# Optimization experiments

Measured on AMD Instinct MI355X. Metric: run time of the kernel, lower is better.

## Reference

```python
import jax, jax.numpy as jnp
import numpy as np

K = 11          # kernel_size
SIGMA = 1.5
CH = 3          # image channels


def _gaussian_kernel(ch):
    coords = jnp.arange(K, dtype=jnp.float32) - (K - 1) / 2
    g = jnp.exp(-coords ** 2 / (2 * SIGMA ** 2))
    g = g / g.sum()
    k2d = jnp.outer(g, g)                       # [K, K]
    return jnp.tile(k2d[None, None], (ch, 1, 1, 1))  # [C, 1, K, K] depthwise


def setup_inputs() -> dict:
    key = jax.random.key(0)
    kx, ky = jax.random.split(key)
    x = jax.random.normal(kx, (32, CH, 512, 512), dtype=jnp.float32)
    y = jax.random.normal(ky, (32, CH, 512, 512), dtype=jnp.float32)
    kernel = _gaussian_kernel(CH)
    return {"x": x, "y": y, "kernel": kernel}


def _blur(v, kernel):
    # depthwise 2D Gaussian blur, SAME padding (K odd)
    c = v.shape[1]
    pad = K // 2
    return jax.lax.conv_general_dilated(
        v, kernel, window_strides=(1, 1), padding=[(pad, pad), (pad, pad)],
        dimension_numbers=("NCHW", "OIHW", "NCHW"), feature_group_count=c)


def reference(x, y, kernel):
    C1 = 0.01 ** 2
    C2 = 0.03 ** 2
    mu_x = _blur(x, kernel)
    mu_y = _blur(y, kernel)
    sigma_x = _blur(x * x, kernel) - mu_x ** 2
    sigma_y = _blur(y * y, kernel) - mu_y ** 2
    sigma_xy = _blur(x * y, kernel) - mu_x * mu_y
    ssim_num = (2 * mu_x * mu_y + C1) * (2 * sigma_xy + C2)
    ssim_den = (mu_x ** 2 + mu_y ** 2 + C1) * (sigma_x + sigma_y + C2)
    ssim = ssim_num / (ssim_den + 1e-8)
    return ((1.0 - ssim) / 2.0).mean()
```

## Files before the change

kernel.cpp:

```cpp
#include <hip/hip_runtime.h>
#include <hip/hip_bf16.h>

#define IMG    512
#define KSZ    11
#define HALO   5
#define STRIP  64
#define PANEL  16
#define NSTEP  32
#define PAIRS  37
#define FSTR32 44
#define FROW   704
#define RSTR32 340

typedef short bf16x8 __attribute__((ext_vector_type(8)));
typedef float f32x4  __attribute__((ext_vector_type(4)));
union S8 { bf16x8 v; ushort u16[8]; uint u32[4]; };

__device__ __forceinline__ uint cvtpk(float lo, float hi) {
    uint r;
    asm("v_cvt_pk_bf16_f32 %0, %1, %2" : "=v"(r) : "v"(lo), "v"(hi));
    return r;
}
__device__ __forceinline__ float2 pk_mul(float2 a, float2 b) {
    float2 d;
    asm("v_pk_mul_f32 %0, %1, %2" : "=v"(d) : "v"(a), "v"(b));
    return d;
}
__device__ __forceinline__ ushort f2bf(float f) {
    union { __hip_bfloat16 h; ushort u; } c;
    c.h = __float2bfloat16(f);
    return c.u;
}


__global__ __launch_bounds__(256)
void dssim_mfma_kernel(const float* __restrict__ x,
                       const float* __restrict__ y,
                       const float* __restrict__ kern,
                       float* __restrict__ out)
{
    __shared__ float  sgf[16];
    __shared__ ushort gext[64];
    __shared__ uint   Fbuf32[5 * FROW];
    __shared__ uint   Ring32[24 * RSTR32];
    __shared__ float  wsum[4];

    const int tid = threadIdx.x;
    const int l   = tid & 63;
    const int wv  = tid >> 6;
    const int q   = l >> 4;
    const int cj  = l & 15;
    const int wcb = wv * 16 + cj;

    if (tid < KSZ) {
        float s = 0.f;
        #pragma unroll
        for (int j = 0; j < KSZ; ++j) s += kern[tid * KSZ + j];
        sgf[tid] = s;
    }
    for (int i = tid; i < 5 * FROW; i += 256) Fbuf32[i] = 0u;
    for (int i = tid; i < 3 * RSTR32; i += 256) Ring32[i] = 0u;
    __syncthreads();
    if (tid < 64) {
        const int d = tid - 16;
        gext[tid] = (d >= 0 && d < KSZ) ? f2bf(sgf[d]) : (ushort)0;
    }
    __syncthreads();

    S8 tgh, tgv;
    #pragma unroll
    for (int ii = 0; ii < 8; ++ii) {
        tgh.u16[ii] = gext[16 + q * 8 + ii - cj];
        tgv.u16[ii] = gext[15 + q * 8 + ii - cj];
    }

    const int plane  = blockIdx.z;
    const int cstrip = blockIdx.x * STRIP;
    const int base   = plane * (IMG * IMG);

    const int srow = tid >> 4;
    const int sp   = tid & 15;
    int gcol0[3], gcol1[3], wo[3];
    bool ok0[3], ok1[3];
    #pragma unroll
    for (int m = 0; m < 3; ++m) {
        const int p  = sp + 16 * m;
        const bool pa = (p < PAIRS);
        const int c0 = cstrip - HALO + 2 * p;
        gcol0[m] = c0;  gcol1[m] = c0 + 1;
        ok0[m] = pa && (c0 >= 0) && (c0 < IMG);
        ok1[m] = pa && (c0 + 1 >= 0) && (c0 + 1 < IMG);
        wo[m]  = srow * FSTR32 + p;
    }
    float2 px[3], py[3];

    auto prefetch = [&](int pn) {
        const int r    = pn * PANEL + srow;
        const bool rok = (r < IMG);
        const int rb   = base + r * IMG;
        #pragma unroll
        for (int m = 0; m < 3; ++m) {
            float a0 = 0.f, a1 = 0.f, b0 = 0.f, b1 = 0.f;
            if (rok && ok0[m]) { a0 = x[rb + gcol0[m]]; b0 = y[rb + gcol0[m]]; }
            if (rok && ok1[m]) { a1 = x[rb + gcol1[m]]; b1 = y[rb + gcol1[m]]; }
            px[m] = make_float2(a0, a1);
            py[m] = make_float2(b0, b1);
        }
    };
    auto commit = [&]() {
        #pragma unroll
        for (int m = 0; m < 3; ++m) {
            if (m < 2 || sp < PAIRS - 32) {
                const float2 vx = px[m], vy = py[m];
                const float2 xx = pk_mul(vx, vx);
                const float2 yy = pk_mul(vy, vy);
                const float2 xy = pk_mul(vx, vy);
                Fbuf32[0 * FROW + wo[m]] = cvtpk(vx.x, vx.y);
                Fbuf32[1 * FROW + wo[m]] = cvtpk(vy.x, vy.y);
                Fbuf32[2 * FROW + wo[m]] = cvtpk(xx.x, xx.y);
                Fbuf32[3 * FROW + wo[m]] = cvtpk(yy.x, yy.y);
                Fbuf32[4 * FROW + wo[m]] = cvtpk(xy.x, xy.y);
            }
        }
    };

    prefetch(0);
    commit();
    __syncthreads();

    const f32x4 z0 = {0.f, 0.f, 0.f, 0.f};
    const float C1 = 1e-4f, C2 = 9e-4f;
    const int aoff = cj * FSTR32 + wv * 8 + q * 4;
    float local = 0.f;
    int hb = 0, vb = 16;

    for (int t = 0; t <= NSTEP; ++t) {
        {
            int p0 = hb + 2 * q + 3;  if (p0 >= 24) p0 -= 24;
            int p1 = p0 + 1;          if (p1 >= 24) p1 -= 24;
            const int rw0 = p0 * RSTR32 + wcb;
            const int rw1 = p1 * RSTR32 + wcb;
            #pragma unroll
            for (int f = 0; f < 5; ++f) {
                S8 a;
                a.v = *(const bf16x8*)&Fbuf32[f * FROW + aoff];
                f32x4 d = __builtin_amdgcn_mfma_f32_16x16x32_bf16(a.v, tgh.v, z0, 0, 0, 0);
                Ring32[rw0 + f * 68] = cvtpk(d[0], d[1]);
                Ring32[rw1 + f * 68] = cvtpk(d[2], d[3]);
            }
        }

        if (t < NSTEP) prefetch(t + 1);

        __syncthreads();

        if (t >= 1) {
            int vr[4];
            #pragma unroll
            for (int ii = 0; ii < 4; ++ii) {
                int pp = vb + 4 * q + ii;  if (pp >= 24) pp -= 24;
                vr[ii] = pp * RSTR32 + wcb;
            }
            f32x4 vf[5];
            #pragma unroll
            for (int f = 0; f < 5; ++f) {
                S8 b;
                #pragma unroll
                for (int ii = 0; ii < 4; ++ii) b.u32[ii] = Ring32[vr[ii] + f * 68];
                vf[f] = __builtin_amdgcn_mfma_f32_16x16x32_bf16(tgv.v, b.v, z0, 0, 0, 0);
            }
            #pragma unroll
            for (int r = 0; r < 4; ++r) {
                const float mx  = vf[0][r], my  = vf[1][r];
                const float exx = vf[2][r], eyy = vf[3][r], exy = vf[4][r];
                const float sxv = fmaf(-mx, mx, exx);
                const float syv = fmaf(-my, my, eyy);
                const float sxy = fmaf(-mx, my, exy);
                const float num = fmaf(2.f, mx * my, C1) * fmaf(2.f, sxy, C2);
                const float den = fmaf(mx, mx, fmaf(my, my, C1)) * (sxv + syv + C2);
                const float ssim = __fdividef(num, den + 1e-8f);
                local += (1.f - ssim) * 0.5f;
            }
        }

        if (t < NSTEP) commit();
        __syncthreads();

        vb = hb;
        hb += 8;  if (hb >= 24) hb -= 24;
    }

    #pragma unroll
    for (int o = 32; o > 0; o >>= 1) local += __shfl_down(local, o, 64);
    if (l == 0) wsum[wv] = local;
    __syncthreads();
    if (tid == 0) {
        const float s = wsum[0] + wsum[1] + wsum[2] + wsum[3];
        atomicAdd(out, s * (1.f / 25165824.f));
    }
}

extern "C" void kernel_launch(void* const* d_in, const int* in_sizes, int n_in,
                              void* d_out, int out_size, void* d_ws, size_t ws_size,
                              hipStream_t stream)
{
    const float* x    = (const float*)d_in[0];
    const float* y    = (const float*)d_in[1];
    const float* kern = (const float*)d_in[2];
    float* out = (float*)d_out;

    hipMemsetAsync(out, 0, sizeof(float), stream);

    dim3 grid(IMG / STRIP, 1, 32 * 3);
    dssim_mfma_kernel<<<grid, 256, 0, stream>>>(x, y, kern, out);
}
```

Before: 81.54 us.

## Feed MFMA A-operand from registers via vector loads and split image rows in halves

Removes the Fbuf shared-memory staging buffer: each lane now loads 8 contiguous floats of x and y with 128-bit vector loads and builds the bf16 A-fragments for the horizontal MFMA directly in registers. The Gaussian tap offsets are shifted to match the new column mapping, which uses a strip start 8 columns earlier. The grid doubles along y so each block processes half the rows, with one overlapping panel to refill the vertical ring. This cuts LDS traffic and a sync-heavy commit phase and raises parallelism, at the cost of some redundant halo panel loads and changed edge handling; colok zeroes whole 8-column groups at image borders.

```diff
diff --git a/kernel.cpp b/kernel.cpp
--- a/kernel.cpp
+++ b/kernel.cpp
@@ -6,11 +6,8 @@
 #define HALO   5
 #define STRIP  64
 #define PANEL  16
-#define NSTEP  32
-#define PAIRS  37
-#define FSTR32 44
-#define FROW   704
-#define RSTR32 340
+#define RSTR32 330
+#define FOFF   66
 
 typedef short bf16x8 __attribute__((ext_vector_type(8)));
 typedef float f32x4  __attribute__((ext_vector_type(4)));
@@ -41,7 +38,6 @@
 {
     __shared__ float  sgf[16];
     __shared__ ushort gext[64];
-    __shared__ uint   Fbuf32[5 * FROW];
     __shared__ uint   Ring32[24 * RSTR32];
     __shared__ float  wsum[4];
 
@@ -58,11 +54,10 @@
         for (int j = 0; j < KSZ; ++j) s += kern[tid * KSZ + j];
         sgf[tid] = s;
     }
-    for (int i = tid; i < 5 * FROW; i += 256) Fbuf32[i] = 0u;
     for (int i = tid; i < 3 * RSTR32; i += 256) Ring32[i] = 0u;
     __syncthreads();
     if (tid < 64) {
-        const int d = tid - 16;
+        const int d = tid - 18;
         gext[tid] = (d >= 0 && d < KSZ) ? f2bf(sgf[d]) : (ushort)0;
     }
     __syncthreads();
@@ -70,91 +65,94 @@
     S8 tgh, tgv;
     #pragma unroll
     for (int ii = 0; ii < 8; ++ii) {
-        tgh.u16[ii] = gext[16 + q * 8 + ii - cj];
-        tgv.u16[ii] = gext[15 + q * 8 + ii - cj];
+        tgh.u16[ii] = gext[15 + q * 8 + ii - cj];
+        tgv.u16[ii] = gext[17 + q * 8 + ii - cj];
     }
 
     const int plane  = blockIdx.z;
+    const int half   = blockIdx.y;
     const int cstrip = blockIdx.x * STRIP;
     const int base   = plane * (IMG * IMG);
 
-    const int srow = tid >> 4;
-    const int sp   = tid & 15;
-    int gcol0[3], gcol1[3], wo[3];
-    bool ok0[3], ok1[3];
-    #pragma unroll
-    for (int m = 0; m < 3; ++m) {
-        const int p  = sp + 16 * m;
-        const bool pa = (p < PAIRS);
-        const int c0 = cstrip - HALO + 2 * p;
-        gcol0[m] = c0;  gcol1[m] = c0 + 1;
-        ok0[m] = pa && (c0 >= 0) && (c0 < IMG);
-        ok1[m] = pa && (c0 + 1 >= 0) && (c0 + 1 < IMG);
-        wo[m]  = srow * FSTR32 + p;
-    }
-    float2 px[3], py[3];
-
-    auto prefetch = [&](int pn) {
-        const int r    = pn * PANEL + srow;
-        const bool rok = (r < IMG);
-        const int rb   = base + r * IMG;
-        #pragma unroll
-        for (int m = 0; m < 3; ++m) {
-            float a0 = 0.f, a1 = 0.f, b0 = 0.f, b1 = 0.f;
-            if (rok && ok0[m]) { a0 = x[rb + gcol0[m]]; b0 = y[rb + gcol0[m]]; }
-            if (rok && ok1[m]) { a1 = x[rb + gcol1[m]]; b1 = y[rb + gcol1[m]]; }
-            px[m] = make_float2(a0, a1);
-            py[m] = make_float2(b0, b1);
+    const int  cb    = cstrip - 8 + 16 * wv + 8 * q;
+    const bool colok = (cb >= 0) && (cb + 8 <= IMG);
+    const float* xp  = x + base + cb;
+    const float* yp  = y + base + cb;
+
+    const int t0   = half ? 15 : 0;
+    const int t1   = half ? 32 : 16;
+    const int vmin = half ? 17 : 1;
+
+    f32x4 xa, xb, ya, yb;
+    auto load8 = [&](int t) {
+        const int r = t * PANEL + cj;
+        if (r < IMG && colok) {
+            const float* px = xp + r * IMG;
+            const float* py = yp + r * IMG;
+            xa = *(const f32x4*)px;  xb = *(const f32x4*)(px + 4);
+            ya = *(const f32x4*)py;  yb = *(const f32x4*)(py + 4);
+        } else {
+            const f32x4 zz = {0.f, 0.f, 0.f, 0.f};
+            xa = zz; xb = zz; ya = zz; yb = zz;
         }
     };
-    auto commit = [&]() {
-        #pragma unroll
-        for (int m = 0; m < 3; ++m) {
-            if (m < 2 || sp < PAIRS - 32) {
-                const float2 vx = px[m], vy = py[m];
-                const float2 xx = pk_mul(vx, vx);
-                const float2 yy = pk_mul(vy, vy);
-                const float2 xy = pk_mul(vx, vy);
-                Fbuf32[0 * FROW + wo[m]] = cvtpk(vx.x, vx.y);
-                Fbuf32[1 * FROW + wo[m]] = cvtpk(vy.x, vy.y);
-                Fbuf32[2 * FROW + wo[m]] = cvtpk(xx.x, xx.y);
-                Fbuf32[3 * FROW + wo[m]] = cvtpk(yy.x, yy.y);
-                Fbuf32[4 * FROW + wo[m]] = cvtpk(xy.x, xy.y);
-            }
-        }
-    };
-
-    prefetch(0);
-    commit();
-    __syncthreads();
+
+    load8(t0);
 
     const f32x4 z0 = {0.f, 0.f, 0.f, 0.f};
     const float C1 = 1e-4f, C2 = 9e-4f;
-    const int aoff = cj * FSTR32 + wv * 8 + q * 4;
     float local = 0.f;
-    int hb = 0, vb = 16;
-
-    for (int t = 0; t <= NSTEP; ++t) {
+    int hb = (8 * t0) % 24;
+
+    for (int t = t0; t <= t1; ++t) {
+        float2 x01 = {xa[0], xa[1]}, x23 = {xa[2], xa[3]};
+        float2 x45 = {xb[0], xb[1]}, x67 = {xb[2], xb[3]};
+        float2 y01 = {ya[0], ya[1]}, y23 = {ya[2], ya[3]};
+        float2 y45 = {yb[0], yb[1]}, y67 = {yb[2], yb[3]};
+        S8 fx, fy, fxx, fyy, fxy;
+        #pragma unroll
+        for (int w = 0; w < 4; ++w) {
+            const float2 xv = (w == 0) ? x01 : (w == 1) ? x23 : (w == 2) ? x45 : x67;
+            const float2 yv = (w == 0) ? y01 : (w == 1) ? y23 : (w == 2) ? y45 : y67;
+            const float2 xxv = pk_mul(xv, xv);
+            const float2 yyv = pk_mul(yv, yv);
+            const float2 xyv = pk_mul(xv, yv);
+            fx .u32[w] = cvtpk(xv.x,  xv.y);
+            fy .u32[w] = cvtpk(yv.x,  yv.y);
+            fxx.u32[w] = cvtpk(xxv.x, xxv.y);
+            fyy.u32[w] = cvtpk(yyv.x, yyv.y);
+            fxy.u32[w] = cvtpk(xyv.x, xyv.y);
+        }
+
+        if (t < t1) load8(t + 1);
+
         {
             int p0 = hb + 2 * q + 3;  if (p0 >= 24) p0 -= 24;
             int p1 = p0 + 1;          if (p1 >= 24) p1 -= 24;
             const int rw0 = p0 * RSTR32 + wcb;
             const int rw1 = p1 * RSTR32 + wcb;
-            #pragma unroll
-            for (int f = 0; f < 5; ++f) {
-                S8 a;
-                a.v = *(const bf16x8*)&Fbuf32[f * FROW + aoff];
-                f32x4 d = __builtin_amdgcn_mfma_f32_16x16x32_bf16(a.v, tgh.v, z0, 0, 0, 0);
-                Ring32[rw0 + f * 68] = cvtpk(d[0], d[1]);
-                Ring32[rw1 + f * 68] = cvtpk(d[2], d[3]);
-            }
-        }
-
-        if (t < NSTEP) prefetch(t + 1);
+            f32x4 d;
+            d = __builtin_amdgcn_mfma_f32_16x16x32_bf16(fx.v,  tgh.v, z0, 0, 0, 0);
+            Ring32[rw0 + 0 * FOFF] = cvtpk(d[0], d[1]);
+            Ring32[rw1 + 0 * FOFF] = cvtpk(d[2], d[3]);
+            d = __builtin_amdgcn_mfma_f32_16x16x32_bf16(fy.v,  tgh.v, z0, 0, 0, 0);
+            Ring32[rw0 + 1 * FOFF] = cvtpk(d[0], d[1]);
+            Ring32[rw1 + 1 * FOFF] = cvtpk(d[2], d[3]);
+            d = __builtin_amdgcn_mfma_f32_16x16x32_bf16(fxx.v, tgh.v, z0, 0, 0, 0);
+            Ring32[rw0 + 2 * FOFF] = cvtpk(d[0], d[1]);
+            Ring32[rw1 + 2 * FOFF] = cvtpk(d[2], d[3]);
+            d = __builtin_amdgcn_mfma_f32_16x16x32_bf16(fyy.v, tgh.v, z0, 0, 0, 0);
+            Ring32[rw0 + 3 * FOFF] = cvtpk(d[0], d[1]);
+            Ring32[rw1 + 3 * FOFF] = cvtpk(d[2], d[3]);
+            d = __builtin_amdgcn_mfma_f32_16x16x32_bf16(fxy.v, tgh.v, z0, 0, 0, 0);
+            Ring32[rw0 + 4 * FOFF] = cvtpk(d[0], d[1]);
+            Ring32[rw1 + 4 * FOFF] = cvtpk(d[2], d[3]);
+        }
 
         __syncthreads();
 
-        if (t >= 1) {
+        if (t >= vmin) {
+            const int vb = (hb >= 8) ? hb - 8 : hb + 16;
             int vr[4];
             #pragma unroll
             for (int ii = 0; ii < 4; ++ii) {
@@ -166,7 +164,7 @@
             for (int f = 0; f < 5; ++f) {
                 S8 b;
                 #pragma unroll
-                for (int ii = 0; ii < 4; ++ii) b.u32[ii] = Ring32[vr[ii] + f * 68];
+                for (int ii = 0; ii < 4; ++ii) b.u32[ii] = Ring32[vr[ii] + f * FOFF];
                 vf[f] = __builtin_amdgcn_mfma_f32_16x16x32_bf16(tgv.v, b.v, z0, 0, 0, 0);
             }
             #pragma unroll
@@ -183,10 +181,8 @@
             }
         }
 
-        if (t < NSTEP) commit();
         __syncthreads();
 
-        vb = hb;
         hb += 8;  if (hb >= 24) hb -= 24;
     }
 
@@ -211,6 +207,6 @@
 
     hipMemsetAsync(out, 0, sizeof(float), stream);
 
-    dim3 grid(IMG / STRIP, 1, 32 * 3);
+    dim3 grid(IMG / STRIP, 2, 32 * 3);
     dssim_mfma_kernel<<<grid, 256, 0, stream>>>(x, y, kern, out);
 }
```

Measured after the change: 81.38 us. About the same (-0.2%).
